# Kernel optimization log

Hardware: AMD Instinct MI355X
Metric: run time of the kernel (lower is better)

## Reference

```python
import jax, jax.numpy as jnp
import numpy as np

B, LQ, LT, D = 16, 576, 512, 768
H, DH = 12, 64
TOPK = 64
GATE_INIT = -4.0
EPS = 1e-5


def _layernorm(x, g, b):
    m = jnp.mean(x, axis=-1, keepdims=True)
    v = jnp.mean(jnp.square(x - m), axis=-1, keepdims=True)
    return (x - m) * jax.lax.rsqrt(v + EPS) * g + b


def setup_inputs() -> dict:
    key = jax.random.key(0)
    ks = jax.random.split(key, 8)
    s = D ** -0.5
    return {
        "x_q": jax.random.normal(ks[0], (B, LQ, D), jnp.float32),
        "x_kv": jax.random.normal(ks[1], (B, LT, D), jnp.float32),
        "kv_attn_mask": jnp.ones((B, LT), jnp.int32),
        "wq": jax.random.normal(ks[2], (D, D), jnp.float32) * s,
        "wk": jax.random.normal(ks[3], (D, D), jnp.float32) * s,
        "wv": jax.random.normal(ks[4], (D, D), jnp.float32) * s,
        "wo": jax.random.normal(ks[5], (D, D), jnp.float32) * s,
        "ln_q_g": jnp.ones((D,), jnp.float32),
        "ln_q_b": jnp.zeros((D,), jnp.float32),
        "ln_kv_g": jnp.ones((D,), jnp.float32),
        "ln_kv_b": jnp.zeros((D,), jnp.float32),
        "head_queries": jax.random.normal(ks[6], (H, DH), jnp.float32) * DH ** -0.5,
        "resid_logit": jnp.asarray(GATE_INIT, jnp.float32),
    }


def reference(x_q, x_kv, kv_attn_mask, wq, wk, wv, wo,
              ln_q_g, ln_q_b, ln_kv_g, ln_kv_b, head_queries, resid_logit):
    scale = DH ** -0.5
    Bc, Lq, _ = x_q.shape
    Lt = x_kv.shape[1]
    xq_n = _layernorm(x_q, ln_q_g, ln_q_b)
    xkv_n = _layernorm(x_kv, ln_kv_g, ln_kv_b)
    # torch Linear: y = x @ W.T
    q = (xq_n @ wq.T).reshape(Bc, Lq, H, DH).transpose(0, 2, 1, 3)   # [B,H,Lq,DH]
    k = (xkv_n @ wk.T).reshape(Bc, Lt, H, DH).transpose(0, 2, 1, 3)  # [B,H,Lt,DH]
    v = (xkv_n @ wv.T).reshape(Bc, Lt, H, DH).transpose(0, 2, 1, 3)

    valid = (kv_attn_mask != 0)  # [B,Lt]
    neg = jnp.asarray(-jnp.inf, q.dtype)

    # head-wise gate from learned head queries attending over keys
    gate_scores = jnp.einsum('hd,bhld->bhl', head_queries, k) * scale  # [B,H,Lt]
    gate_scores = jnp.where(valid[:, None, :], gate_scores, neg)
    gate_attn = jax.nn.softmax(gate_scores, axis=-1)
    c_h = jnp.einsum('bhl,bhld->bhd', gate_attn, k)
    g_logits = jnp.einsum('bhd,hd->bh', c_h, head_queries) * scale
    g_h = jax.nn.sigmoid(g_logits)[:, :, None, None]  # [B,H,1,1]

    # top-k token routing: zero out non-selected K/V (matches torch.where -> zeros)
    if TOPK and TOPK < Lt:
        _, topk_idx = jax.lax.top_k(gate_scores, TOPK)  # [B,H,K]
        keep = jax.nn.one_hot(topk_idx, Lt, dtype=q.dtype).sum(axis=-2) > 0  # [B,H,Lt]
        k = jnp.where(keep[..., None], k, 0.0)
        v = jnp.where(keep[..., None], v, 0.0)

    attn_logits = jnp.einsum('bhqd,bhkd->bhqk', q, k) * scale  # [B,H,Lq,Lt]
    attn_logits = jnp.where(valid[:, None, None, :], attn_logits, neg)
    attn = jax.nn.softmax(attn_logits, axis=-1)
    out = jnp.einsum('bhqk,bhkd->bhqd', attn, v) * g_h
    out = out.transpose(0, 2, 1, 3).reshape(Bc, Lq, H * DH)
    out = out @ wo.T
    alpha = jax.nn.sigmoid(resid_logit)
    return x_q + alpha * out
```

## Files before the change

### kernel.cpp

```cpp
#include <hip/hip_runtime.h>
#include <math.h>

#define BB 16
#define LQ 576
#define LT 512
#define DD 768
#define HH 12
#define DH 64
#define TOPK 64

typedef __attribute__((ext_vector_type(8))) short bf16x8;
typedef __attribute__((ext_vector_type(4))) float f32x4;
typedef __attribute__((ext_vector_type(4))) unsigned short u16x4;

static constexpr size_t XQBF  = 0;
static constexpr size_t XKVBF = 3538944;
static constexpr size_t WQB   = 6684672;
static constexpr size_t WKB   = 6979584;
static constexpr size_t WVB   = 7274496;
static constexpr size_t WOB   = 7569408;
static constexpr size_t QBFo  = 7864320;
static constexpr size_t UBo   = 11403264;
static constexpr size_t GSo   = 11409408;
static constexpr size_t IDXo  = 17694720;
static constexpr size_t VBIA  = 17707008;
static constexpr size_t NDVo  = 17719296;
static constexpr size_t GHo   = 17719488;
static constexpr size_t KCo   = 17719680;
static constexpr size_t VCTo  = 18112896;

__device__ inline unsigned short f2bf(float f) {
  union { float f; unsigned u; } v; v.f = f;
  unsigned r = v.u + 0x7FFFu + ((v.u >> 16) & 1u);
  return (unsigned short)(r >> 16);
}
__device__ inline float bf2f(unsigned short u) {
  union { unsigned u; float f; } v; v.u = ((unsigned)u) << 16;
  return v.f;
}
__device__ inline void gload_lds16(const void* src, void* dst) {
  __builtin_amdgcn_global_load_lds((const __attribute__((address_space(1))) void*)src,
                                   (__attribute__((address_space(3))) void*)dst, 16, 0, 0);
}
__device__ inline bf16x8 lds_read16(const unsigned short* p) {
  bf16x8 r;
  asm volatile("ds_read_b128 %0, %1"
               : "=v"(r)
               : "v"((const __attribute__((address_space(3))) unsigned short*)p));
  return r;
}

__global__ __launch_bounds__(256) void ln_all(const float* __restrict__ xq,
                                              const float* __restrict__ xkv,
                                              const float* __restrict__ gq,
                                              const float* __restrict__ bq,
                                              const float* __restrict__ gkv,
                                              const float* __restrict__ bkv,
                                              unsigned short* __restrict__ yq,
                                              unsigned short* __restrict__ ykv) {
  int row = blockIdx.x;
  const float *xr, *gg, *bb;
  unsigned short* yr;
  if (row < BB * LQ) {
    xr = xq + (size_t)row * DD; gg = gq; bb = bq; yr = yq + (size_t)row * DD;
  } else {
    int r = row - BB * LQ;
    xr = xkv + (size_t)r * DD; gg = gkv; bb = bkv; yr = ykv + (size_t)r * DD;
  }
  int t = threadIdx.x;
  float v0 = xr[t], v1 = xr[t + 256], v2 = xr[t + 512];
  __shared__ float red[4];
  float s = v0 + v1 + v2;
  #pragma unroll
  for (int o = 32; o > 0; o >>= 1) s += __shfl_xor(s, o);
  if ((t & 63) == 0) red[t >> 6] = s;
  __syncthreads();
  float m = (red[0] + red[1] + red[2] + red[3]) * (1.0f / 768.0f);
  float d0 = v0 - m, d1 = v1 - m, d2 = v2 - m;
  float s2 = d0 * d0 + d1 * d1 + d2 * d2;
  #pragma unroll
  for (int o = 32; o > 0; o >>= 1) s2 += __shfl_xor(s2, o);
  __syncthreads();
  if ((t & 63) == 0) red[t >> 6] = s2;
  __syncthreads();
  float var = (red[0] + red[1] + red[2] + red[3]) * (1.0f / 768.0f);
  float rs = rsqrtf(var + 1e-5f);
  yr[t]       = f2bf(d0 * rs * gg[t]       + bb[t]);
  yr[t + 256] = f2bf(d1 * rs * gg[t + 256] + bb[t + 256]);
  yr[t + 512] = f2bf(d2 * rs * gg[t + 512] + bb[t + 512]);
}

__global__ __launch_bounds__(256) void conv4u(const float* __restrict__ s0, const float* __restrict__ s1,
                                              const float* __restrict__ s2, const float* __restrict__ s3,
                                              unsigned short* d0, unsigned short* d1,
                                              unsigned short* d2, unsigned short* d3,
                                              const float* __restrict__ hq,
                                              unsigned short* __restrict__ UB) {
  int t = threadIdx.x;
  if (blockIdx.y == 4) {
    int h = blockIdx.x;
    if (h >= 16) return;
    if (h < HH) {
      float a0 = 0.0f, a1 = 0.0f, a2 = 0.0f;
      for (int d = 0; d < DH; ++d) {
        float sc = hq[h * DH + d];
        const float* wr = s1 + (size_t)(h * DH + d) * DD;
        a0 += sc * wr[t]; a1 += sc * wr[t + 256]; a2 += sc * wr[t + 512];
      }
      UB[h * DD + t]       = f2bf(a0 * 0.125f);
      UB[h * DD + t + 256] = f2bf(a1 * 0.125f);
      UB[h * DD + t + 512] = f2bf(a2 * 0.125f);
    } else {
      UB[h * DD + t] = 0; UB[h * DD + t + 256] = 0; UB[h * DD + t + 512] = 0;
    }
    return;
  }
  const float* s; unsigned short* d;
  switch (blockIdx.y) {
    case 0: s = s0; d = d0; break;
    case 1: s = s1; d = d1; break;
    case 2: s = s2; d = d2; break;
    default: s = s3; d = d3; break;
  }
  int i = (blockIdx.x * 256 + t) * 4;
  float4 v = *reinterpret_cast<const float4*>(&s[i]);
  u16x4 o = { f2bf(v.x), f2bf(v.y), f2bf(v.z), f2bf(v.w) };
  *reinterpret_cast<u16x4*>(&d[i]) = o;
}


#define COMMON_PREAMBLE()                                                      \
  const int tid = threadIdx.x;                                                 \
  const int w = tid >> 6, l = tid & 63;                                        \
  const int lq = l & 15, g = l >> 4;                                           \
  const int srow = l >> 3;                                                     \
  const int scol = ((l & 7) * 16) ^ ((srow & 7) << 4);

#define STAGE2(BUFI, T)                                                        \
  {                                                                            \
    int k0s = (T) * 64;                                                        \
    _Pragma("unroll")                                                          \
    for (int it = 0; it < 4; ++it) {                                           \
      int rbase = it * 32 + w * 8;                                             \
      gload_lds16(Asrc + (size_t)rbase * DD + k0s, &As[BUFI][rbase * 64]);     \
      gload_lds16(Bsrc + (size_t)rbase * DD + k0s, &Bs[BUFI][rbase * 64]);     \
    }                                                                          \
  }

#define COMPUTE2(BUFI)                                                         \
  {                                                                            \
    bf16x8 a[4][2], b[4][2];                                                   \
    _Pragma("unroll")                                                          \
    for (int mi = 0; mi < 4; ++mi)                                             \
      _Pragma("unroll")                                                        \
      for (int ks = 0; ks < 2; ++ks) {                                         \
        a[mi][ks] = lds_read16(&As[BUFI][aoff[mi][ks]]);                       \
        b[mi][ks] = lds_read16(&Bs[BUFI][boff[mi][ks]]);                       \
      }                                                                        \
    asm volatile("s_waitcnt lgkmcnt(0)" ::: "memory");                         \
    __builtin_amdgcn_sched_barrier(0);                                         \
    _Pragma("unroll")                                                          \
    for (int ks = 0; ks < 2; ++ks)                                             \
      _Pragma("unroll")                                                        \
      for (int mi = 0; mi < 4; ++mi)                                           \
        _Pragma("unroll")                                                      \
        for (int ni = 0; ni < 4; ++ni)                                         \
          acc[mi][ni] = __builtin_amdgcn_mfma_f32_16x16x32_bf16(               \
              a[mi][ks], b[ni][ks], acc[mi][ni], 0, 0, 0);                     \
  }

#define GEMM_MAIN()                                                            \
  int aoff[4][2], boff[4][2];                                                  \
  _Pragma("unroll")                                                            \
  for (int mi = 0; mi < 4; ++mi) {                                             \
    int rowa = wr * 64 + mi * 16 + lq;                                         \
    int rowb = wc * 64 + mi * 16 + lq;                                         \
    _Pragma("unroll")                                                          \
    for (int ks = 0; ks < 2; ++ks) {                                           \
      aoff[mi][ks] = rowa * 64 + (((ks * 64 + g * 16) ^ ((rowa & 7) << 4)) >> 1); \
      boff[mi][ks] = rowb * 64 + (((ks * 64 + g * 16) ^ ((rowb & 7) << 4)) >> 1); \
    }                                                                          \
  }                                                                            \
  STAGE2(0, 0);                                                                \
  STAGE2(1, 1);                                                                \
  _Pragma("unroll")                                                            \
  for (int t = 0; t < 12; ++t) {                                               \
    if (t < 11) asm volatile("s_waitcnt vmcnt(8)" ::: "memory");               \
    else        asm volatile("s_waitcnt vmcnt(0)" ::: "memory");               \
    __builtin_amdgcn_sched_barrier(0);                                         \
    __builtin_amdgcn_s_barrier();                                              \
    if ((t & 1) == 0) { COMPUTE2(0); } else { COMPUTE2(1); }                   \
    __builtin_amdgcn_s_barrier();                                              \
    __builtin_amdgcn_sched_barrier(0);                                         \
    if (t + 2 < 12) {                                                          \
      if ((t & 1) == 0) { STAGE2(0, t + 2); } else { STAGE2(1, t + 2); }       \
    }                                                                          \
  }

__global__ __launch_bounds__(256) void gs_gemm(const unsigned short* __restrict__ xkvb,
                                               const unsigned short* __restrict__ UB,
                                               float* __restrict__ GS) {
  __shared__ __align__(16) unsigned short Xs[2][64 * 64];
  __shared__ __align__(16) unsigned short Us[2][16 * 64];
  COMMON_PREAMBLE();
  const int bm = blockIdx.x * 64;
  const unsigned short* Asrc = xkvb + (size_t)(bm + srow) * DD + (scol >> 1);
  const unsigned short* Us0 = UB + (size_t)srow * DD + (scol >> 1);
  const unsigned short* Us1 = UB + (size_t)(8 + srow) * DD + (scol >> 1);

#define GS_STAGE(BUFI, T)                                                      \
  {                                                                            \
    int k0s = (T) * 64;                                                        \
    _Pragma("unroll")                                                          \
    for (int it = 0; it < 2; ++it) {                                           \
      int rbase = it * 32 + w * 8;                                             \
      gload_lds16(Asrc + (size_t)rbase * DD + k0s, &Xs[BUFI][rbase * 64]);     \
    }                                                                          \
    gload_lds16(Us0 + k0s, &Us[BUFI][0]);                                      \
    gload_lds16(Us1 + k0s, &Us[BUFI][8 * 64]);                                 \
  }

  f32x4 acc = {};

#define GS_COMPUTE(BUFI)                                                       \
  {                                                                            \
    bf16x8 a[2], b[2];                                                         \
    _Pragma("unroll")                                                          \
    for (int ks = 0; ks < 2; ++ks) {                                           \
      int arow = w * 16 + lq;                                                  \
      int acb = (ks * 64 + g * 16) ^ ((arow & 7) << 4);                        \
      a[ks] = lds_read16(&Xs[BUFI][arow * 64 + (acb >> 1)]);                   \
      int brow = lq;                                                           \
      int bcb = (ks * 64 + g * 16) ^ ((brow & 7) << 4);                        \
      b[ks] = lds_read16(&Us[BUFI][brow * 64 + (bcb >> 1)]);                   \
    }                                                                          \
    asm volatile("s_waitcnt lgkmcnt(0)" ::: "memory");                         \
    __builtin_amdgcn_sched_barrier(0);                                         \
    _Pragma("unroll")                                                          \
    for (int ks = 0; ks < 2; ++ks)                                             \
      acc = __builtin_amdgcn_mfma_f32_16x16x32_bf16(a[ks], b[ks], acc, 0, 0, 0); \
  }

  GS_STAGE(0, 0);
  GS_STAGE(1, 1);
  #pragma unroll
  for (int t = 0; t < 12; ++t) {
    if (t < 11) asm volatile("s_waitcnt vmcnt(4)" ::: "memory");
    else        asm volatile("s_waitcnt vmcnt(0)" ::: "memory");
    __builtin_amdgcn_sched_barrier(0);
    __builtin_amdgcn_s_barrier();
    if ((t & 1) == 0) { GS_COMPUTE(0); } else { GS_COMPUTE(1); }
    __builtin_amdgcn_s_barrier();
    __builtin_amdgcn_sched_barrier(0);
    if (t + 2 < 12) {
      if ((t & 1) == 0) { GS_STAGE(0, t + 2); } else { GS_STAGE(1, t + 2); }
    }
  }
  #pragma unroll
  for (int r = 0; r < 4; ++r)
    GS[(size_t)(bm + w * 16 + g * 4 + r) * 16 + lq] = acc[r];
}

__global__ __launch_bounds__(512) void gate_topk(const float* __restrict__ GS,
                                                 const int* __restrict__ mask,
                                                 int* __restrict__ idxo,
                                                 float* __restrict__ vbias,
                                                 float* __restrict__ ndv,
                                                 float* __restrict__ g_h) {
  int bh = blockIdx.x, b = bh / HH, h = bh % HH;
  int l = threadIdx.x;
  __shared__ float s_sc[512];
  __shared__ float red[8];
  __shared__ int wred[8];
  float sc = GS[(size_t)(b * LT + l) * 16 + h];
  bool maskv = (mask[b * LT + l] != 0);
  if (!maskv) sc = -INFINITY;
  s_sc[l] = sc;
  float m0 = sc;
  #pragma unroll
  for (int o = 32; o > 0; o >>= 1) m0 = fmaxf(m0, __shfl_xor(m0, o));
  if ((l & 63) == 0) red[l >> 6] = m0;
  __syncthreads();
  float m = red[0];
  #pragma unroll
  for (int w = 1; w < 8; w++) m = fmaxf(m, red[w]);
  float p = __expf(sc - m);
  float s1 = p;
  #pragma unroll
  for (int o = 32; o > 0; o >>= 1) s1 += __shfl_xor(s1, o);
  __syncthreads();
  if ((l & 63) == 0) red[l >> 6] = s1;
  __syncthreads();
  float Z = 0.0f;
  #pragma unroll
  for (int w = 0; w < 8; w++) Z += red[w];
  p /= Z;
  float gc = maskv ? p * sc : 0.0f;
  #pragma unroll
  for (int o = 32; o > 0; o >>= 1) gc += __shfl_xor(gc, o);
  __syncthreads();
  if ((l & 63) == 0) red[l >> 6] = gc;
  __syncthreads();
  if (l == 0) {
    float G = 0.0f;
    #pragma unroll
    for (int w = 0; w < 8; w++) G += red[w];
    g_h[bh] = 1.0f / (1.0f + __expf(-G));
  }
  float my = s_sc[l];
  int cnt = 0;
  for (int j = 0; j < LT; j++) {
    float sj = s_sc[j];
    cnt += (sj > my || (sj == my && j < l)) ? 1 : 0;
  }
  if (cnt < TOPK) {
    idxo[bh * TOPK + cnt] = l;
    vbias[bh * TOPK + cnt] = maskv ? 0.0f : -INFINITY;
  }
  int dv = (maskv && cnt >= TOPK) ? 1 : 0;
  unsigned long long bal = __ballot(dv);
  if ((l & 63) == 0) wred[l >> 6] = __popcll(bal);
  __syncthreads();
  if (l == 0) {
    int nd = 0;
    #pragma unroll
    for (int w = 0; w < 8; w++) nd += wred[w];
    ndv[bh] = (float)nd;
  }
}

__global__ __launch_bounds__(256, 2) void proj2(const unsigned short* __restrict__ xqb,
                                                const unsigned short* __restrict__ wqb,
                                                const unsigned short* __restrict__ xkvb,
                                                const unsigned short* __restrict__ wkb,
                                                const unsigned short* __restrict__ wvb,
                                                const int* __restrict__ idxo,
                                                unsigned short* __restrict__ QBF,
                                                unsigned short* __restrict__ KC,
                                                unsigned short* __restrict__ VCT) {
  __shared__ __align__(16) unsigned short As[2][128 * 64];
  __shared__ __align__(16) unsigned short Bs[2][128 * 64];
  __shared__ int sidx[64];
  COMMON_PREAMBLE();
  int p = blockIdx.x;
  int bid = (p & 7) * 78 + (p >> 3);

  if (bid < 432) {
    const int wr = w >> 1, wc = w & 1;
    const int mtile = bid / 6, nt = bid % 6;
    const int bm = mtile * 128, bn = nt * 128;
    const unsigned short* Asrc = xqb + (size_t)(bm + srow) * DD + (scol >> 1);
    const unsigned short* Bsrc = wqb + (size_t)(bn + srow) * DD + (scol >> 1);
    f32x4 acc[4][4] = {};
    GEMM_MAIN();
    const int m_base = bm + wr * 64, n_base = bn + wc * 64;
    #pragma unroll
    for (int mi = 0; mi < 4; ++mi)
      #pragma unroll
      for (int r = 0; r < 4; ++r) {
        int m = m_base + mi * 16 + g * 4 + r;
        #pragma unroll
        for (int ni = 0; ni < 4; ++ni) {
          int n = n_base + ni * 16 + lq;
          QBF[(size_t)m * DD + n] = f2bf(acc[mi][ni][r] * 0.125f);
        }
      }
  } else {
    const int bh = bid - 432, b = bh / HH, h = bh % HH;
    if (tid < 64) sidx[tid] = idxo[bh * TOPK + tid];
    __syncthreads();
    unsigned short* Xs0 = &As[0][0]; unsigned short* Xs1 = &As[0][4096];
    unsigned short* Kp0 = &As[1][0]; unsigned short* Kp1 = &As[1][4096];
    unsigned short* Vp0 = &Bs[0][0]; unsigned short* Vp1 = &Bs[0][4096];
    const int j0 = w * 16 + srow, j1 = w * 16 + 8 + srow;
    const unsigned short* xs0 = xkvb + (size_t)(b * LT + sidx[j0]) * DD + (scol >> 1);
    const unsigned short* xs1 = xkvb + (size_t)(b * LT + sidx[j1]) * DD + (scol >> 1);
    const unsigned short* wk0 = wkb + (size_t)(h * DH + j0) * DD + (scol >> 1);
    const unsigned short* wk1 = wkb + (size_t)(h * DH + j1) * DD + (scol >> 1);
    const unsigned short* wv0 = wvb + (size_t)(h * DH + j0) * DD + (scol >> 1);
    const unsigned short* wv1 = wvb + (size_t)(h * DH + j1) * DD + (scol >> 1);

#define KV_STAGE(Xd, Kd, Vd, T)                                                \
    {                                                                          \
      int k0s = (T) * 64;                                                      \
      gload_lds16(xs0 + k0s, Xd + (w * 16) * 64);                              \
      gload_lds16(xs1 + k0s, Xd + (w * 16 + 8) * 64);                          \
      gload_lds16(wk0 + k0s, Kd + (w * 16) * 64);                              \
      gload_lds16(wk1 + k0s, Kd + (w * 16 + 8) * 64);                          \
      gload_lds16(wv0 + k0s, Vd + (w * 16) * 64);                              \
      gload_lds16(wv1 + k0s, Vd + (w * 16 + 8) * 64);                          \
    }

    f32x4 accK[4] = {}, accV[4] = {};

#define KV_COMPUTE(Xd, Kd, Vd)                                                 \
    {                                                                          \
      bf16x8 ax[2], av[2], bk[4][2], bx[4][2];                                 \
      _Pragma("unroll")                                                        \
      for (int ks = 0; ks < 2; ++ks) {                                         \
        int arow = w * 16 + lq;                                                \
        int acb = (ks * 64 + g * 16) ^ ((arow & 7) << 4);                      \
        ax[ks] = lds_read16(Xd + arow * 64 + (acb >> 1));                      \
        av[ks] = lds_read16(Vd + arow * 64 + (acb >> 1));                      \
        _Pragma("unroll")                                                      \
        for (int ni = 0; ni < 4; ++ni) {                                       \
          int brow = ni * 16 + lq;                                             \
          int bcb = (ks * 64 + g * 16) ^ ((brow & 7) << 4);                    \
          bk[ni][ks] = lds_read16(Kd + brow * 64 + (bcb >> 1));                \
          bx[ni][ks] = lds_read16(Xd + brow * 64 + (bcb >> 1));                \
        }                                                                      \
      }                                                                        \
      asm volatile("s_waitcnt lgkmcnt(0)" ::: "memory");                       \
      __builtin_amdgcn_sched_barrier(0);                                       \
      _Pragma("unroll")                                                        \
      for (int ks = 0; ks < 2; ++ks)                                           \
        _Pragma("unroll")                                                      \
        for (int ni = 0; ni < 4; ++ni) {                                       \
          accK[ni] = __builtin_amdgcn_mfma_f32_16x16x32_bf16(ax[ks], bk[ni][ks], accK[ni], 0, 0, 0); \
          accV[ni] = __builtin_amdgcn_mfma_f32_16x16x32_bf16(av[ks], bx[ni][ks], accV[ni], 0, 0, 0); \
        }                                                                      \
    }

    KV_STAGE(Xs0, Kp0, Vp0, 0);
    KV_STAGE(Xs1, Kp1, Vp1, 1);
    #pragma unroll
    for (int t = 0; t < 12; ++t) {
      if (t < 11) asm volatile("s_waitcnt vmcnt(6)" ::: "memory");
      else        asm volatile("s_waitcnt vmcnt(0)" ::: "memory");
      __builtin_amdgcn_sched_barrier(0);
      __builtin_amdgcn_s_barrier();
      if ((t & 1) == 0) { KV_COMPUTE(Xs0, Kp0, Vp0); } else { KV_COMPUTE(Xs1, Kp1, Vp1); }
      __builtin_amdgcn_s_barrier();
      __builtin_amdgcn_sched_barrier(0);
      if (t + 2 < 12) {
        if ((t & 1) == 0) { KV_STAGE(Xs0, Kp0, Vp0, t + 2); } else { KV_STAGE(Xs1, Kp1, Vp1, t + 2); }
      }
    }
    #pragma unroll
    for (int ni = 0; ni < 4; ++ni)
      #pragma unroll
      for (int r = 0; r < 4; ++r) {
        int mrow = w * 16 + g * 4 + r;
        KC [(size_t)bh * 4096 + mrow * 64 + ni * 16 + lq] = f2bf(accK[ni][r]);
        VCT[(size_t)bh * 4096 + mrow * 64 + ni * 16 + lq] = f2bf(accV[ni][r]);
      }
  }
}

__global__ __launch_bounds__(256, 2) void o_gemm(const unsigned short* __restrict__ ABF,
                                                 const unsigned short* __restrict__ wob,
                                                 float* __restrict__ out,
                                                 const float* __restrict__ resid,
                                                 const float* __restrict__ gl) {
  __shared__ __align__(16) unsigned short As[2][128 * 64];
  __shared__ __align__(16) unsigned short Bs[2][128 * 64];
  COMMON_PREAMBLE();
  const int wr = w >> 1, wc = w & 1;
  int p = blockIdx.x;
  int bid = (p & 7) * 54 + (p >> 3);
  const int mtile = bid / 6, nt = bid % 6;
  const int bm = mtile * 128, bn = nt * 128;
  const unsigned short* Asrc = ABF + (size_t)(bm + srow) * DD + (scol >> 1);
  const unsigned short* Bsrc = wob + (size_t)(bn + srow) * DD + (scol >> 1);

  f32x4 acc[4][4] = {};
  GEMM_MAIN();

  float alpha = 1.0f / (1.0f + __expf(-gl[0]));
  const int m_base = bm + wr * 64, n_base = bn + wc * 64;
  #pragma unroll
  for (int mi = 0; mi < 4; ++mi)
    #pragma unroll
    for (int r = 0; r < 4; ++r) {
      int m = m_base + mi * 16 + g * 4 + r;
      #pragma unroll
      for (int ni = 0; ni < 4; ++ni) {
        int n = n_base + ni * 16 + lq;
        out[(size_t)m * DD + n] = resid[(size_t)m * DD + n] + alpha * acc[mi][ni][r];
      }
    }
}

__global__ __launch_bounds__(256) void attn_topk(const unsigned short* __restrict__ Qb,
                                                 const unsigned short* __restrict__ KC,
                                                 const unsigned short* __restrict__ VCT,
                                                 const float* __restrict__ vbias,
                                                 const float* __restrict__ ndv,
                                                 const float* __restrict__ g_h,
                                                 unsigned short* __restrict__ att) {
  const int bh = blockIdx.y, b = bh / HH, h = bh % HH;
  const int q0 = blockIdx.x * 64;
  const int tid = threadIdx.x;
  const int w = tid >> 6, l = tid & 63;
  const int lq = l & 15, g = l >> 4;

  __shared__ __align__(16) unsigned short Klds[64 * 64];
  __shared__ __align__(16) unsigned short Vlds[64 * 64];
  __shared__ float svb[64];

  const int srow = l >> 3;
  const int scol = ((l & 7) * 16) ^ ((srow & 7) << 4);
  #pragma unroll
  for (int it = 0; it < 2; ++it) {
    int rbase = w * 16 + it * 8;
    gload_lds16(KC  + (size_t)bh * 4096 + (rbase + srow) * 64 + (scol >> 1), &Klds[rbase * 64]);
    gload_lds16(VCT + (size_t)bh * 4096 + (rbase + srow) * 64 + (scol >> 1), &Vlds[rbase * 64]);
  }
  if (tid < 64) svb[tid] = vbias[bh * TOPK + tid];

  bf16x8 qf0, qf1;
  {
    const unsigned short* qrow =
        Qb + ((size_t)(b * LQ + q0 + w * 16 + lq)) * DD + h * DH + g * 8;
    qf0 = *reinterpret_cast<const bf16x8*>(qrow);
    qf1 = *reinterpret_cast<const bf16x8*>(qrow + 32);
  }
  __syncthreads();

  f32x4 S[4];
  #pragma unroll
  for (int kt = 0; kt < 4; ++kt) {
    f32x4 acc = {};
    int row = kt * 16 + lq;
    int c0 = (g * 16) ^ ((row & 7) << 4);
    int c1 = (64 + g * 16) ^ ((row & 7) << 4);
    bf16x8 a0 = *reinterpret_cast<const bf16x8*>(&Klds[row * 64 + (c0 >> 1)]);
    bf16x8 a1 = *reinterpret_cast<const bf16x8*>(&Klds[row * 64 + (c1 >> 1)]);
    acc = __builtin_amdgcn_mfma_f32_16x16x32_bf16(a0, qf0, acc, 0, 0, 0);
    acc = __builtin_amdgcn_mfma_f32_16x16x32_bf16(a1, qf1, acc, 0, 0, 0);
    S[kt] = acc;
  }

  float s_v[16];
  float mx = -INFINITY;
  #pragma unroll
  for (int kt = 0; kt < 4; ++kt)
    #pragma unroll
    for (int r = 0; r < 4; ++r) {
      float s = S[kt][r] + svb[kt * 16 + g * 4 + r];
      s_v[kt * 4 + r] = s;
      mx = fmaxf(mx, s);
    }
  mx = fmaxf(mx, __shfl_xor(mx, 16));
  mx = fmaxf(mx, __shfl_xor(mx, 32));
  float nd = ndv[bh];
  float m2 = (nd > 0.0f) ? fmaxf(mx, 0.0f) : mx;

  float psum = 0.0f;
  unsigned short pb[16];
  #pragma unroll
  for (int i = 0; i < 16; ++i) {
    float p = __expf(s_v[i] - m2);
    psum += p;
    pb[i] = f2bf(p);
  }
  psum += __shfl_xor(psum, 16);
  psum += __shfl_xor(psum, 32);
  float Z = psum + nd * __expf(-m2);
  float inv = 1.0f / Z;

  bf16x8 pa0, pa1;
  #pragma unroll
  for (int j = 0; j < 8; ++j) { pa0[j] = (short)pb[j]; pa1[j] = (short)pb[8 + j]; }

  f32x4 O[4] = {};
  #pragma unroll
  for (int dt = 0; dt < 4; ++dt) {
    int r = dt * 16 + lq;
    int swz = (r & 7) << 4;
    #pragma unroll
    for (int ks = 0; ks < 2; ++ks) {
      int cl = (64 * ks + g * 8) ^ swz;
      int ch = (64 * ks + 32 + g * 8) ^ swz;
      u16x4 lo = *reinterpret_cast<const u16x4*>(&Vlds[r * 64 + (cl >> 1)]);
      u16x4 hi = *reinterpret_cast<const u16x4*>(&Vlds[r * 64 + (ch >> 1)]);
      bf16x8 vb = { (short)lo[0], (short)lo[1], (short)lo[2], (short)lo[3],
                    (short)hi[0], (short)hi[1], (short)hi[2], (short)hi[3] };
      O[dt] = __builtin_amdgcn_mfma_f32_16x16x32_bf16(ks == 0 ? pa0 : pa1, vb, O[dt], 0, 0, 0);
    }
  }

  float invl[4];
  #pragma unroll
  for (int r = 0; r < 4; ++r) invl[r] = __shfl(inv, g * 4 + r);
  float gh = g_h[bh];
  #pragma unroll
  for (int dt = 0; dt < 4; ++dt)
    #pragma unroll
    for (int r = 0; r < 4; ++r) {
      int q = q0 + w * 16 + g * 4 + r;
      att[((size_t)(b * LQ + q)) * DD + h * DH + dt * 16 + lq] =
          f2bf(O[dt][r] * invl[r] * gh);
    }
}

extern "C" void kernel_launch(void* const* d_in, const int* in_sizes, int n_in,
                              void* d_out, int out_size, void* d_ws, size_t ws_size,
                              hipStream_t stream) {
  const float* x_q      = (const float*)d_in[0];
  const float* x_kv     = (const float*)d_in[1];
  const int*   mask     = (const int*)d_in[2];
  const float* wq       = (const float*)d_in[3];
  const float* wk       = (const float*)d_in[4];
  const float* wv       = (const float*)d_in[5];
  const float* wo       = (const float*)d_in[6];
  const float* ln_q_g   = (const float*)d_in[7];
  const float* ln_q_b   = (const float*)d_in[8];
  const float* ln_kv_g  = (const float*)d_in[9];
  const float* ln_kv_b  = (const float*)d_in[10];
  const float* hq       = (const float*)d_in[11];
  const float* resid_l  = (const float*)d_in[12];
  float* out = (float*)d_out;
  float* ws  = (float*)d_ws;

  unsigned short* xqb  = (unsigned short*)(ws + XQBF);
  unsigned short* xkvb = (unsigned short*)(ws + XKVBF);
  unsigned short* wqb  = (unsigned short*)(ws + WQB);
  unsigned short* wkb  = (unsigned short*)(ws + WKB);
  unsigned short* wvb  = (unsigned short*)(ws + WVB);
  unsigned short* wob  = (unsigned short*)(ws + WOB);
  unsigned short* QBF  = (unsigned short*)(ws + QBFo);
  unsigned short* UB   = (unsigned short*)(ws + UBo);
  float*          GS   = (float*)(ws + GSo);
  int*            IDX  = (int*)(ws + IDXo);
  unsigned short* KC   = (unsigned short*)(ws + KCo);
  unsigned short* VCT  = (unsigned short*)(ws + VCTo);
  unsigned short* ABF  = xqb;

  conv4u<<<dim3(576, 5), dim3(256), 0, stream>>>(wq, wk, wv, wo, wqb, wkb, wvb, wob, hq, UB);

  ln_all<<<dim3(BB * LQ + BB * LT), dim3(256), 0, stream>>>(x_q, x_kv, ln_q_g, ln_q_b,
                                                            ln_kv_g, ln_kv_b, xqb, xkvb);

  gs_gemm<<<dim3(128), dim3(256), 0, stream>>>(xkvb, UB, GS);

  gate_topk<<<dim3(BB * HH), dim3(512), 0, stream>>>(GS, mask, IDX,
                                                     ws + VBIA, ws + NDVo, ws + GHo);

  proj2<<<dim3(624), dim3(256), 0, stream>>>(xqb, wqb, xkvb, wkb, wvb, IDX, QBF, KC, VCT);

  attn_topk<<<dim3(LQ / 64, BB * HH), dim3(256), 0, stream>>>(QBF, KC, VCT,
                                                              ws + VBIA, ws + NDVo, ws + GHo, ABF);

  o_gemm<<<dim3(432), dim3(256), 0, stream>>>(ABF, wob, out, x_q, resid_l);
}
```

Measured before the change: 103.1 us.

## Switch GEMMs to 3-stage K=32 LDS pipeline with smaller shared footprint

Replaces the double-buffered K=64 tiles in the projection and output GEMMs with a triple-buffered K=32 pipeline using a new XOR swizzle. Shared memory per block drops from 64KB to 48KB, so the launch bounds are raised to allow three blocks per CU. The aim is more latency hiding through deeper prefetch and higher occupancy. In exchange there are twice as many barrier-synchronized iterations, fewer MFMAs per barrier, and more register pressure under the higher occupancy target.

```diff
diff --git a/kernel.cpp b/kernel.cpp
--- a/kernel.cpp
+++ b/kernel.cpp
@@ -128,7 +128,6 @@
   *reinterpret_cast<u16x4*>(&d[i]) = o;
 }
 
-
 #define COMMON_PREAMBLE()                                                      \
   const int tid = threadIdx.x;                                                 \
   const int w = tid >> 6, l = tid & 63;                                        \
@@ -136,65 +135,60 @@
   const int srow = l >> 3;                                                     \
   const int scol = ((l & 7) * 16) ^ ((srow & 7) << 4);
 
-#define STAGE2(BUFI, T)                                                        \
+
+#define Q32_STAGE(T)                                                           \
   {                                                                            \
-    int k0s = (T) * 64;                                                        \
+    int k0s = (T) * 32;                                                        \
+    unsigned short* Ad = S + ((T) % 3) * 4096;                                 \
+    unsigned short* Bd = S + 12288 + ((T) % 3) * 4096;                         \
+    gload_lds16(Asrc0 + k0s, Ad + (w * 32) * 32);                              \
+    gload_lds16(Asrc1 + k0s, Ad + (w * 32 + 16) * 32);                         \
+    gload_lds16(Bsrc0 + k0s, Bd + (w * 32) * 32);                              \
+    gload_lds16(Bsrc1 + k0s, Bd + (w * 32 + 16) * 32);                         \
+  }
+
+#define Q32_COMPUTE(T)                                                         \
+  {                                                                            \
+    const unsigned short* Ab = S + ((T) % 3) * 4096;                           \
+    const unsigned short* Bb = S + 12288 + ((T) % 3) * 4096;                   \
+    bf16x8 a[4], b[4];                                                         \
     _Pragma("unroll")                                                          \
-    for (int it = 0; it < 4; ++it) {                                           \
-      int rbase = it * 32 + w * 8;                                             \
-      gload_lds16(Asrc + (size_t)rbase * DD + k0s, &As[BUFI][rbase * 64]);     \
-      gload_lds16(Bsrc + (size_t)rbase * DD + k0s, &Bs[BUFI][rbase * 64]);     \
-    }                                                                          \
-  }
-
-#define COMPUTE2(BUFI)                                                         \
-  {                                                                            \
-    bf16x8 a[4][2], b[4][2];                                                   \
+    for (int mi = 0; mi < 4; ++mi)                                             \
+      a[mi] = lds_read16(Ab + (wr * 64 + mi * 16 + lq) * 32 + gsw);            \
+    _Pragma("unroll")                                                          \
+    for (int ni = 0; ni < 4; ++ni)                                             \
+      b[ni] = lds_read16(Bb + (wc * 64 + ni * 16 + lq) * 32 + gsw);            \
+    asm volatile("s_waitcnt lgkmcnt(0)" ::: "memory");                         \
+    __builtin_amdgcn_sched_barrier(0);                                         \
     _Pragma("unroll")                                                          \
     for (int mi = 0; mi < 4; ++mi)                                             \
       _Pragma("unroll")                                                        \
-      for (int ks = 0; ks < 2; ++ks) {                                         \
-        a[mi][ks] = lds_read16(&As[BUFI][aoff[mi][ks]]);                       \
-        b[mi][ks] = lds_read16(&Bs[BUFI][boff[mi][ks]]);                       \
-      }                                                                        \
-    asm volatile("s_waitcnt lgkmcnt(0)" ::: "memory");                         \
-    __builtin_amdgcn_sched_barrier(0);                                         \
-    _Pragma("unroll")                                                          \
-    for (int ks = 0; ks < 2; ++ks)                                             \
-      _Pragma("unroll")                                                        \
-      for (int mi = 0; mi < 4; ++mi)                                           \
-        _Pragma("unroll")                                                      \
-        for (int ni = 0; ni < 4; ++ni)                                         \
-          acc[mi][ni] = __builtin_amdgcn_mfma_f32_16x16x32_bf16(               \
-              a[mi][ks], b[ni][ks], acc[mi][ni], 0, 0, 0);                     \
-  }
-
-#define GEMM_MAIN()                                                            \
-  int aoff[4][2], boff[4][2];                                                  \
+      for (int ni = 0; ni < 4; ++ni)                                           \
+        acc[mi][ni] = __builtin_amdgcn_mfma_f32_16x16x32_bf16(                 \
+            a[mi], b[ni], acc[mi][ni], 0, 0, 0);                               \
+  }
+
+#define Q32_MAIN(APTR, WPTR)                                                   \
+  const int wr = w >> 1, wc = w & 1;                                           \
+  const int selem = ((l & 3) ^ ((l >> 3) & 3)) * 8;                            \
+  const int gsw = (g ^ ((lq >> 1) & 3)) * 8;                                   \
+  const unsigned short* Asrc0 = (APTR) + (size_t)(bm + w * 32 + (l >> 2)) * DD + selem; \
+  const unsigned short* Asrc1 = Asrc0 + (size_t)16 * DD;                       \
+  const unsigned short* Bsrc0 = (WPTR) + (size_t)(bn + w * 32 + (l >> 2)) * DD + selem; \
+  const unsigned short* Bsrc1 = Bsrc0 + (size_t)16 * DD;                       \
+  f32x4 acc[4][4] = {};                                                        \
+  Q32_STAGE(0); Q32_STAGE(1); Q32_STAGE(2);                                    \
   _Pragma("unroll")                                                            \
-  for (int mi = 0; mi < 4; ++mi) {                                             \
-    int rowa = wr * 64 + mi * 16 + lq;                                         \
-    int rowb = wc * 64 + mi * 16 + lq;                                         \
-    _Pragma("unroll")                                                          \
-    for (int ks = 0; ks < 2; ++ks) {                                           \
-      aoff[mi][ks] = rowa * 64 + (((ks * 64 + g * 16) ^ ((rowa & 7) << 4)) >> 1); \
-      boff[mi][ks] = rowb * 64 + (((ks * 64 + g * 16) ^ ((rowb & 7) << 4)) >> 1); \
-    }                                                                          \
-  }                                                                            \
-  STAGE2(0, 0);                                                                \
-  STAGE2(1, 1);                                                                \
-  _Pragma("unroll")                                                            \
-  for (int t = 0; t < 12; ++t) {                                               \
-    if (t < 11) asm volatile("s_waitcnt vmcnt(8)" ::: "memory");               \
-    else        asm volatile("s_waitcnt vmcnt(0)" ::: "memory");               \
+  for (int t = 0; t < 24; ++t) {                                               \
+    if (t < 22)       asm volatile("s_waitcnt vmcnt(8)" ::: "memory");         \
+    else if (t == 22) asm volatile("s_waitcnt vmcnt(4)" ::: "memory");         \
+    else              asm volatile("s_waitcnt vmcnt(0)" ::: "memory");         \
     __builtin_amdgcn_sched_barrier(0);                                         \
     __builtin_amdgcn_s_barrier();                                              \
-    if ((t & 1) == 0) { COMPUTE2(0); } else { COMPUTE2(1); }                   \
+    Q32_COMPUTE(t);                                                            \
     __builtin_amdgcn_s_barrier();                                              \
     __builtin_amdgcn_sched_barrier(0);                                         \
-    if (t + 2 < 12) {                                                          \
-      if ((t & 1) == 0) { STAGE2(0, t + 2); } else { STAGE2(1, t + 2); }       \
-    }                                                                          \
+    if (t + 3 < 24) Q32_STAGE(t + 3);                                          \
   }
 
 __global__ __launch_bounds__(256) void gs_gemm(const unsigned short* __restrict__ xkvb,
@@ -329,7 +323,7 @@
   }
 }
 
-__global__ __launch_bounds__(256, 2) void proj2(const unsigned short* __restrict__ xqb,
+__global__ __launch_bounds__(256, 3) void proj2(const unsigned short* __restrict__ xqb,
                                                 const unsigned short* __restrict__ wqb,
                                                 const unsigned short* __restrict__ xkvb,
                                                 const unsigned short* __restrict__ wkb,
@@ -338,21 +332,17 @@
                                                 unsigned short* __restrict__ QBF,
                                                 unsigned short* __restrict__ KC,
                                                 unsigned short* __restrict__ VCT) {
-  __shared__ __align__(16) unsigned short As[2][128 * 64];
-  __shared__ __align__(16) unsigned short Bs[2][128 * 64];
+  __shared__ __align__(16) unsigned short S[24576];
   __shared__ int sidx[64];
   COMMON_PREAMBLE();
+  (void)srow; (void)scol;
   int p = blockIdx.x;
   int bid = (p & 7) * 78 + (p >> 3);
 
   if (bid < 432) {
-    const int wr = w >> 1, wc = w & 1;
     const int mtile = bid / 6, nt = bid % 6;
     const int bm = mtile * 128, bn = nt * 128;
-    const unsigned short* Asrc = xqb + (size_t)(bm + srow) * DD + (scol >> 1);
-    const unsigned short* Bsrc = wqb + (size_t)(bn + srow) * DD + (scol >> 1);
-    f32x4 acc[4][4] = {};
-    GEMM_MAIN();
+    Q32_MAIN(xqb, wqb);
     const int m_base = bm + wr * 64, n_base = bn + wc * 64;
     #pragma unroll
     for (int mi = 0; mi < 4; ++mi)
@@ -369,72 +359,59 @@
     const int bh = bid - 432, b = bh / HH, h = bh % HH;
     if (tid < 64) sidx[tid] = idxo[bh * TOPK + tid];
     __syncthreads();
-    unsigned short* Xs0 = &As[0][0]; unsigned short* Xs1 = &As[0][4096];
-    unsigned short* Kp0 = &As[1][0]; unsigned short* Kp1 = &As[1][4096];
-    unsigned short* Vp0 = &Bs[0][0]; unsigned short* Vp1 = &Bs[0][4096];
-    const int j0 = w * 16 + srow, j1 = w * 16 + 8 + srow;
-    const unsigned short* xs0 = xkvb + (size_t)(b * LT + sidx[j0]) * DD + (scol >> 1);
-    const unsigned short* xs1 = xkvb + (size_t)(b * LT + sidx[j1]) * DD + (scol >> 1);
-    const unsigned short* wk0 = wkb + (size_t)(h * DH + j0) * DD + (scol >> 1);
-    const unsigned short* wk1 = wkb + (size_t)(h * DH + j1) * DD + (scol >> 1);
-    const unsigned short* wv0 = wvb + (size_t)(h * DH + j0) * DD + (scol >> 1);
-    const unsigned short* wv1 = wvb + (size_t)(h * DH + j1) * DD + (scol >> 1);
-
-#define KV_STAGE(Xd, Kd, Vd, T)                                                \
+    const int selem = ((l & 3) ^ ((l >> 3) & 3)) * 8;
+    const int gsw = (g ^ ((lq >> 1) & 3)) * 8;
+    const unsigned short* xsr = xkvb + (size_t)(b * LT + sidx[w * 16 + (l >> 2)]) * DD + selem;
+    const unsigned short* wkr = wkb + (size_t)(h * DH + w * 16 + (l >> 2)) * DD + selem;
+    const unsigned short* wvr = wvb + (size_t)(h * DH + w * 16 + (l >> 2)) * DD + selem;
+
+#define KV32_STAGE(T)                                                          \
     {                                                                          \
-      int k0s = (T) * 64;                                                      \
-      gload_lds16(xs0 + k0s, Xd + (w * 16) * 64);                              \
-      gload_lds16(xs1 + k0s, Xd + (w * 16 + 8) * 64);                          \
-      gload_lds16(wk0 + k0s, Kd + (w * 16) * 64);                              \
-      gload_lds16(wk1 + k0s, Kd + (w * 16 + 8) * 64);                          \
-      gload_lds16(wv0 + k0s, Vd + (w * 16) * 64);                              \
-      gload_lds16(wv1 + k0s, Vd + (w * 16 + 8) * 64);                          \
+      int k0s = (T) * 32;                                                      \
+      unsigned short* Xd = S + ((T) % 3) * 2048;                               \
+      unsigned short* Kd = S + 6144 + ((T) % 3) * 2048;                        \
+      unsigned short* Vd = S + 12288 + ((T) % 3) * 2048;                       \
+      gload_lds16(xsr + k0s, Xd + (w * 16) * 32);                              \
+      gload_lds16(wkr + k0s, Kd + (w * 16) * 32);                              \
+      gload_lds16(wvr + k0s, Vd + (w * 16) * 32);                              \
     }
 
     f32x4 accK[4] = {}, accV[4] = {};
 
-#define KV_COMPUTE(Xd, Kd, Vd)                                                 \
+#define KV32_COMPUTE(T)                                                        \
     {                                                                          \
-      bf16x8 ax[2], av[2], bk[4][2], bx[4][2];                                 \
+      const unsigned short* Xb = S + ((T) % 3) * 2048;                         \
+      const unsigned short* Kb2 = S + 6144 + ((T) % 3) * 2048;                 \
+      const unsigned short* Vb2 = S + 12288 + ((T) % 3) * 2048;                \
+      bf16x8 ax = lds_read16(Xb + (w * 16 + lq) * 32 + gsw);                   \
+      bf16x8 av = lds_read16(Vb2 + (w * 16 + lq) * 32 + gsw);                  \
+      bf16x8 bk[4], bx[4];                                                     \
       _Pragma("unroll")                                                        \
-      for (int ks = 0; ks < 2; ++ks) {                                         \
-        int arow = w * 16 + lq;                                                \
-        int acb = (ks * 64 + g * 16) ^ ((arow & 7) << 4);                      \
-        ax[ks] = lds_read16(Xd + arow * 64 + (acb >> 1));                      \
-        av[ks] = lds_read16(Vd + arow * 64 + (acb >> 1));                      \
-        _Pragma("unroll")                                                      \
-        for (int ni = 0; ni < 4; ++ni) {                                       \
-          int brow = ni * 16 + lq;                                             \
-          int bcb = (ks * 64 + g * 16) ^ ((brow & 7) << 4);                    \
-          bk[ni][ks] = lds_read16(Kd + brow * 64 + (bcb >> 1));                \
-          bx[ni][ks] = lds_read16(Xd + brow * 64 + (bcb >> 1));                \
-        }                                                                      \
+      for (int ni = 0; ni < 4; ++ni) {                                         \
+        bk[ni] = lds_read16(Kb2 + (ni * 16 + lq) * 32 + gsw);                  \
+        bx[ni] = lds_read16(Xb + (ni * 16 + lq) * 32 + gsw);                   \
       }                                                                        \
       asm volatile("s_waitcnt lgkmcnt(0)" ::: "memory");                       \
       __builtin_amdgcn_sched_barrier(0);                                       \
       _Pragma("unroll")                                                        \
-      for (int ks = 0; ks < 2; ++ks)                                           \
-        _Pragma("unroll")                                                      \
-        for (int ni = 0; ni < 4; ++ni) {                                       \
-          accK[ni] = __builtin_amdgcn_mfma_f32_16x16x32_bf16(ax[ks], bk[ni][ks], accK[ni], 0, 0, 0); \
-          accV[ni] = __builtin_amdgcn_mfma_f32_16x16x32_bf16(av[ks], bx[ni][ks], accV[ni], 0, 0, 0); \
-        }                                                                      \
-    }
-
-    KV_STAGE(Xs0, Kp0, Vp0, 0);
-    KV_STAGE(Xs1, Kp1, Vp1, 1);
-    #pragma unroll
-    for (int t = 0; t < 12; ++t) {
-      if (t < 11) asm volatile("s_waitcnt vmcnt(6)" ::: "memory");
-      else        asm volatile("s_waitcnt vmcnt(0)" ::: "memory");
+      for (int ni = 0; ni < 4; ++ni) {                                         \
+        accK[ni] = __builtin_amdgcn_mfma_f32_16x16x32_bf16(ax, bk[ni], accK[ni], 0, 0, 0); \
+        accV[ni] = __builtin_amdgcn_mfma_f32_16x16x32_bf16(av, bx[ni], accV[ni], 0, 0, 0); \
+      }                                                                        \
+    }
+
+    KV32_STAGE(0); KV32_STAGE(1); KV32_STAGE(2);
+    #pragma unroll
+    for (int t = 0; t < 24; ++t) {
+      if (t < 22)       asm volatile("s_waitcnt vmcnt(6)" ::: "memory");
+      else if (t == 22) asm volatile("s_waitcnt vmcnt(3)" ::: "memory");
+      else              asm volatile("s_waitcnt vmcnt(0)" ::: "memory");
       __builtin_amdgcn_sched_barrier(0);
       __builtin_amdgcn_s_barrier();
-      if ((t & 1) == 0) { KV_COMPUTE(Xs0, Kp0, Vp0); } else { KV_COMPUTE(Xs1, Kp1, Vp1); }
+      KV32_COMPUTE(t);
       __builtin_amdgcn_s_barrier();
       __builtin_amdgcn_sched_barrier(0);
-      if (t + 2 < 12) {
-        if ((t & 1) == 0) { KV_STAGE(Xs0, Kp0, Vp0, t + 2); } else { KV_STAGE(Xs1, Kp1, Vp1, t + 2); }
-      }
+      if (t + 3 < 24) KV32_STAGE(t + 3);
     }
     #pragma unroll
     for (int ni = 0; ni < 4; ++ni)
@@ -447,25 +424,19 @@
   }
 }
 
-__global__ __launch_bounds__(256, 2) void o_gemm(const unsigned short* __restrict__ ABF,
+__global__ __launch_bounds__(256, 3) void o_gemm(const unsigned short* __restrict__ ABF,
                                                  const unsigned short* __restrict__ wob,
                                                  float* __restrict__ out,
                                                  const float* __restrict__ resid,
                                                  const float* __restrict__ gl) {
-  __shared__ __align__(16) unsigned short As[2][128 * 64];
-  __shared__ __align__(16) unsigned short Bs[2][128 * 64];
+  __shared__ __align__(16) unsigned short S[24576];
   COMMON_PREAMBLE();
-  const int wr = w >> 1, wc = w & 1;
+  (void)srow; (void)scol;
   int p = blockIdx.x;
   int bid = (p & 7) * 54 + (p >> 3);
   const int mtile = bid / 6, nt = bid % 6;
   const int bm = mtile * 128, bn = nt * 128;
-  const unsigned short* Asrc = ABF + (size_t)(bm + srow) * DD + (scol >> 1);
-  const unsigned short* Bsrc = wob + (size_t)(bn + srow) * DD + (scol >> 1);
-
-  f32x4 acc[4][4] = {};
-  GEMM_MAIN();
-
+  Q32_MAIN(ABF, wob);
   float alpha = 1.0f / (1.0f + __expf(-gl[0]));
   const int m_base = bm + wr * 64, n_base = bn + wc * 64;
   #pragma unroll
```

Result: slower. 107.6 us (+4.4%).
